# Optimization experiments

Measured on AMD Instinct MI355X. Metric: run time of the kernel, lower is better.

## Reference

```python
import jax, jax.numpy as jnp
import numpy as np

SPP_LEVELS = (4, 3, 2, 1)

def spp(x):
    # x: (N, C, H, W); H, W divisible by every level -> exact adaptive max pool
    N, C, H, W = x.shape
    feats = []
    for n in SPP_LEVELS:
        p = x.reshape(N, C, n, H // n, n, W // n).max(axis=(3, 5))  # (N,C,n,n)
        feats.append(p.reshape(N, -1))
    return jnp.concatenate(feats, axis=-1)  # (N, C*30) = (N, 90)

def lstm_cell(x, h, c, Wih, Whh, bih, bhh):
    g = Wih @ x + bih + Whh @ h + bhh
    i, f, gg, o = jnp.split(g, 4)
    i = jax.nn.sigmoid(i); f = jax.nn.sigmoid(f)
    gg = jnp.tanh(gg); o = jax.nn.sigmoid(o)
    c2 = f * c + i * gg
    return o * jnp.tanh(c2), c2

def setup_inputs() -> dict:
    key = jax.random.key(0)
    ks = jax.random.split(key, 16)
    E = 4096
    frames = jax.random.normal(ks[0], (1, 512, 3, 192, 192), dtype=jnp.float32)
    s = 0.02
    return {
        'frames': frames,
        'W_spp': jax.random.normal(ks[1], (E, 90), jnp.float32) * s,
        'b_spp': jnp.zeros((E,), jnp.float32),
        'W_fc7': jax.random.normal(ks[2], (64, E), jnp.float32) * s,
        'b_fc7': jnp.zeros((64,), jnp.float32),
        'W_fcast': jax.random.normal(ks[3], (64, E), jnp.float32) * s,
        'b_fcast': jnp.zeros((64,), jnp.float32),
        'Wih1': jax.random.normal(ks[4], (256, 64), jnp.float32) * s,
        'Whh1': jax.random.normal(ks[5], (256, 64), jnp.float32) * s,
        'bih1': jnp.zeros((256,), jnp.float32),
        'bhh1': jnp.zeros((256,), jnp.float32),
        'Wih2': jax.random.normal(ks[6], (128, 64), jnp.float32) * s,
        'Whh2': jax.random.normal(ks[7], (128, 32), jnp.float32) * s,
        'bih2': jnp.zeros((128,), jnp.float32),
        'bhh2': jnp.zeros((128,), jnp.float32),
        'W_fc8': jax.random.normal(ks[8], (1, 32), jnp.float32) * s,
        'b_fc8': jnp.zeros((1,), jnp.float32),
    }

def reference(frames, W_spp, b_spp, W_fc7, b_fc7, W_fcast, b_fcast,
              Wih1, Whh1, bih1, bhh1, Wih2, Whh2, bih2, bhh2, W_fc8, b_fc8):
    B, S, C, H, W = frames.shape  # B == 1 (module semantics require it)
    flat = frames.reshape(B * S, C, H, W)
    pooled = spp(flat)                                   # (S, 90)
    pooled = jax.nn.relu(pooled @ W_spp.T + b_spp)       # (S, 4096); dropout p=0
    embedded = jax.nn.relu(pooled @ W_fc7.T + b_fc7)     # (S, 64)
    fcast = jax.nn.relu(pooled @ W_fcast.T + b_fcast)    # (S, 64)

    def step(carry, xs):
        h1, c1, h2, c2 = carry
        x, fx = xs
        h1, c1 = lstm_cell(x, h1, c1, Wih1, Whh1, bih1, bhh1)
        h2, c2 = lstm_cell(h1, h2, c2, Wih2, Whh2, bih2, bhh2)
        # forecast branch: same cells with updated hidden, but state not kept
        fh1, _ = lstm_cell(fx, h1, c1, Wih1, Whh1, bih1, bhh1)
        fh2, _ = lstm_cell(fh1, h2, c2, Wih2, Whh2, bih2, bhh2)
        return (h1, c1, h2, c2), (h2, fh2)

    init = (jnp.zeros(64), jnp.zeros(64), jnp.zeros(32), jnp.zeros(32))
    _, (prog, fprog) = jax.lax.scan(step, init, (embedded, fcast))  # (S,32) each

    progress = jax.nn.sigmoid(prog @ W_fc8.T + b_fc8).reshape(B, S)
    forecasted = jax.nn.sigmoid(fprog @ W_fc8.T + b_fc8).reshape(B, S)
    return progress, forecasted
```

## Files before the change

### kernel.cpp

```cpp
#include <hip/hip_runtime.h>
#include <float.h>
#include <math.h>

__global__ __launch_bounds__(192) void spp_kernel(const float* __restrict__ frames,
                                                  float* __restrict__ pooled) {
    int bc = blockIdx.x;
    int w  = threadIdx.x;
    const float* img = frames + (size_t)bc * (192 * 192);

    float cm[12];
#pragma unroll
    for (int ch = 0; ch < 12; ++ch) {
        float m = -FLT_MAX;
#pragma unroll
        for (int r = 0; r < 16; ++r)
            m = fmaxf(m, img[(ch * 16 + r) * 192 + w]);
        cm[ch] = m;
    }

    __shared__ float band[10][192];
#pragma unroll
    for (int i = 0; i < 4; ++i)
        band[i][w] = fmaxf(fmaxf(cm[3*i], cm[3*i+1]), cm[3*i+2]);
#pragma unroll
    for (int i = 0; i < 3; ++i)
        band[4+i][w] = fmaxf(fmaxf(cm[4*i], cm[4*i+1]), fmaxf(cm[4*i+2], cm[4*i+3]));
#pragma unroll
    for (int i = 0; i < 2; ++i) {
        float m = cm[6*i];
#pragma unroll
        for (int k = 1; k < 6; ++k) m = fmaxf(m, cm[6*i+k]);
        band[7+i][w] = m;
    }
    {
        float m = cm[0];
#pragma unroll
        for (int k = 1; k < 12; ++k) m = fmaxf(m, cm[k]);
        band[9][w] = m;
    }
    __syncthreads();

    int s = bc / 3, c = bc % 3;
    float* orow = pooled + s * 90;
    int t = w;
    if (t < 16) {
        int r = t >> 2, cc = t & 3;
        float m = -FLT_MAX;
        for (int x = cc * 48; x < cc * 48 + 48; ++x) m = fmaxf(m, band[r][x]);
        orow[c * 16 + t] = m;
    } else if (t < 25) {
        int idx = t - 16, r = idx / 3, cc = idx % 3;
        float m = -FLT_MAX;
        for (int x = cc * 64; x < cc * 64 + 64; ++x) m = fmaxf(m, band[4 + r][x]);
        orow[48 + c * 9 + idx] = m;
    } else if (t < 29) {
        int idx = t - 25, r = idx >> 1, cc = idx & 1;
        float m = -FLT_MAX;
        for (int x = cc * 96; x < cc * 96 + 96; ++x) m = fmaxf(m, band[7 + r][x]);
        orow[75 + c * 4 + idx] = m;
    } else if (t == 29) {
        float m = -FLT_MAX;
        for (int x = 0; x < 192; ++x) m = fmaxf(m, band[9][x]);
        orow[87 + c] = m;
    }
}

__global__ __launch_bounds__(256) void fc_spp_kernel(const float* __restrict__ pooled,
                                                     const float* __restrict__ W,
                                                     const float* __restrict__ b,
                                                     float* __restrict__ out) {
    int ec = blockIdx.x;
    int fc = blockIdx.y;
    int t  = threadIdx.x;
    int s0 = fc * 8;

    __shared__ __align__(16) float sp[90 * 8];
    for (int i = t; i < 720; i += 256) {
        int j = i >> 3, f = i & 7;
        sp[i] = pooled[(s0 + f) * 90 + j];
    }
    __syncthreads();

    int e0 = ec * 1024 + t;
    float acc[4][8];
#pragma unroll
    for (int k = 0; k < 4; ++k) {
        float bb = b[e0 + k * 256];
#pragma unroll
        for (int f = 0; f < 8; ++f) acc[k][f] = bb;
    }
    for (int j = 0; j < 90; ++j) {
        float w0 = W[(e0 + 0 * 256) * 90 + j];
        float w1 = W[(e0 + 1 * 256) * 90 + j];
        float w2 = W[(e0 + 2 * 256) * 90 + j];
        float w3 = W[(e0 + 3 * 256) * 90 + j];
        float4 pa = *(const float4*)&sp[j * 8 + 0];
        float4 pb = *(const float4*)&sp[j * 8 + 4];
        float pv[8] = {pa.x, pa.y, pa.z, pa.w, pb.x, pb.y, pb.z, pb.w};
#pragma unroll
        for (int f = 0; f < 8; ++f) {
            acc[0][f] += w0 * pv[f];
            acc[1][f] += w1 * pv[f];
            acc[2][f] += w2 * pv[f];
            acc[3][f] += w3 * pv[f];
        }
    }
#pragma unroll
    for (int k = 0; k < 4; ++k)
#pragma unroll
        for (int f = 0; f < 8; ++f)
            out[(size_t)(s0 + f) * 4096 + e0 + k * 256] = fmaxf(acc[k][f], 0.f);
}

__global__ __launch_bounds__(512) void fc7cast_kernel(const float* __restrict__ prelu,
                                                      const float* __restrict__ W7,
                                                      const float* __restrict__ b7,
                                                      const float* __restrict__ Wc,
                                                      const float* __restrict__ bc,
                                                      float* __restrict__ emb,
                                                      float* __restrict__ fca) {
    int blk = blockIdx.x;
    int t   = threadIdx.x;
    int s0  = blk * 4;

    __shared__ __align__(16) float pr[4 * 4096];
    const float4* src = (const float4*)(prelu + (size_t)s0 * 4096);
    float4* dst = (float4*)pr;
    for (int i = t; i < 4096; i += 512) dst[i] = src[i];
    __syncthreads();

    int o = t & 127;
    int f = t >> 7;
    const float* wr;
    float bias;
    if (o < 64) { wr = W7 + (size_t)o * 4096; bias = b7[o]; }
    else        { wr = Wc + (size_t)(o - 64) * 4096; bias = bc[o - 64]; }

    const float4* w4 = (const float4*)wr;
    const float4* p4 = (const float4*)(pr + f * 4096);
    float a0 = 0.f, a1 = 0.f, a2 = 0.f, a3 = 0.f;
    for (int j = 0; j < 1024; ++j) {
        float4 wv = w4[j];
        float4 pv = p4[j];
        a0 += wv.x * pv.x; a1 += wv.y * pv.y;
        a2 += wv.z * pv.z; a3 += wv.w * pv.w;
    }
    float a = fmaxf(a0 + a1 + a2 + a3 + bias, 0.f);
    if (o < 64) emb[(s0 + f) * 64 + o] = a;
    else        fca[(s0 + f) * 64 + (o - 64)] = a;
}

__global__ __launch_bounds__(256) void pregate_kernel(const float* __restrict__ emb,
                                                      const float* __restrict__ fca,
                                                      const float* __restrict__ Wih1,
                                                      const float* __restrict__ bih1,
                                                      const float* __restrict__ bhh1,
                                                      float* __restrict__ gm,
                                                      float* __restrict__ gf) {
    int s = blockIdx.x;
    int t = threadIdx.x;
    __shared__ float x[64], fx[64];
    if (t < 64) x[t] = emb[s * 64 + t];
    else if (t < 128) fx[t - 64] = fca[s * 64 + (t - 64)];
    __syncthreads();

    const float* wr = Wih1 + t * 64;
    float am = bih1[t] + bhh1[t];
    float af = am;
#pragma unroll
    for (int j = 0; j < 64; ++j) {
        float w = wr[j];
        am += w * x[j];
        af += w * fx[j];
    }
    gm[s * 256 + t] = am;
    gf[s * 256 + t] = af;
}

__device__ __forceinline__ float sigf(float x) { return 1.f / (1.f + expf(-x)); }
__device__ __forceinline__ float act_fun(float x, int type) {
    return (type == 2) ? tanhf(x) : sigf(x);
}

__global__ __launch_bounds__(256) void lstm_main_kernel(const float* __restrict__ gm,
                                                        const float* __restrict__ Whh1,
                                                        const float* __restrict__ Wih2,
                                                        const float* __restrict__ Whh2,
                                                        const float* __restrict__ bih2,
                                                        const float* __restrict__ bhh2,
                                                        float* __restrict__ h1t,
                                                        float* __restrict__ c1t,
                                                        float* __restrict__ h2t,
                                                        float* __restrict__ c2t) {
    int t = threadIdx.x;

    __shared__ __align__(16) float h1s[64];
    __shared__ __align__(16) float h2s[32];
    __shared__ float act1[256];
    __shared__ float act2[128];
    __shared__ float act2p[128];

    float wh[64];
#pragma unroll
    for (int j = 0; j < 64; ++j) wh[j] = Whh1[t * 64 + j];

    float wu[64];
#pragma unroll
    for (int j = 0; j < 64; ++j) wu[j] = 0.f;
    float b2 = 0.f;
    if (t < 128) {
#pragma unroll
        for (int j = 0; j < 64; ++j) wu[j] = Wih2[t * 64 + j];
        b2 = bih2[t] + bhh2[t];
    } else {
#pragma unroll
        for (int j = 0; j < 32; ++j) wu[j] = Whh2[(t - 128) * 32 + j];
    }

    float c1r = 0.f;
    float c2r = 0.f;
    if (t < 64) h1s[t] = 0.f;
    if (t < 32) h2s[t] = 0.f;
    __syncthreads();

    float gmv = gm[t];

    for (int s = 0; s < 512; ++s) {
        float gnext = (s < 511) ? gm[(s + 1) * 256 + t] : 0.f;

        {
            float a0 = 0.f, a1 = 0.f, a2 = 0.f, a3 = 0.f;
#pragma unroll
            for (int j = 0; j < 16; ++j) {
                float4 h = ((const float4*)h1s)[j];
                a0 += wh[4*j+0] * h.x; a1 += wh[4*j+1] * h.y;
                a2 += wh[4*j+2] * h.z; a3 += wh[4*j+3] * h.w;
            }
            act1[t] = act_fun(gmv + ((a0 + a1) + (a2 + a3)), t >> 6);
        }
        gmv = gnext;
        __syncthreads();

        if (t < 64) {
            float iv = act1[t], fv = act1[64+t], gv = act1[128+t], ov = act1[192+t];
            float cn = fv * c1r + iv * gv;
            c1r = cn;
            float hn = ov * tanhf(cn);
            h1s[t] = hn;
            h1t[s * 64 + t] = hn;
            c1t[s * 64 + t] = cn;
        }
        __syncthreads();

        if (t < 128) {
            float a0 = b2, a1 = 0.f, a2 = 0.f, a3 = 0.f;
#pragma unroll
            for (int j = 0; j < 16; ++j) {
                float4 h = ((const float4*)h1s)[j];
                a0 += wu[4*j+0] * h.x; a1 += wu[4*j+1] * h.y;
                a2 += wu[4*j+2] * h.z; a3 += wu[4*j+3] * h.w;
            }
            act2[t] = (a0 + a1) + (a2 + a3);
        } else {
            float a0 = 0.f, a1 = 0.f, a2 = 0.f, a3 = 0.f;
#pragma unroll
            for (int j = 0; j < 8; ++j) {
                float4 h = ((const float4*)h2s)[j];
                a0 += wu[4*j+0] * h.x; a1 += wu[4*j+1] * h.y;
                a2 += wu[4*j+2] * h.z; a3 += wu[4*j+3] * h.w;
            }
            act2p[t - 128] = (a0 + a1) + (a2 + a3);
        }
        __syncthreads();

        if (t < 32) {
            float iv = sigf(act2[t]       + act2p[t]);
            float fv = sigf(act2[32 + t]  + act2p[32 + t]);
            float gv = tanhf(act2[64 + t] + act2p[64 + t]);
            float ov = sigf(act2[96 + t]  + act2p[96 + t]);
            float cn = fv * c2r + iv * gv;
            c2r = cn;
            float hn = ov * tanhf(cn);
            h2s[t] = hn;
            h2t[s * 32 + t] = hn;
            c2t[s * 32 + t] = cn;
        }
    }
}

__global__ __launch_bounds__(256) void forecast_kernel(const float* __restrict__ gf,
                                                       const float* __restrict__ Whh1,
                                                       const float* __restrict__ Wih2,
                                                       const float* __restrict__ Whh2,
                                                       const float* __restrict__ bih2,
                                                       const float* __restrict__ bhh2,
                                                       const float* __restrict__ h1t,
                                                       const float* __restrict__ c1t,
                                                       const float* __restrict__ h2t,
                                                       const float* __restrict__ c2t,
                                                       const float* __restrict__ Wfc8,
                                                       const float* __restrict__ bfc8,
                                                       float* __restrict__ out) {
    int s = blockIdx.x;
    int t = threadIdx.x;

    __shared__ __align__(16) float h1v[64];
    __shared__ __align__(16) float h2v[32];
    __shared__ __align__(16) float fh1[64];
    __shared__ float a1s[256];
    __shared__ float a2s[128];

    if (t < 64) h1v[t] = h1t[s * 64 + t];
    else if (t < 96) h2v[t - 64] = h2t[s * 32 + (t - 64)];
    __syncthreads();

    {
        const float* wr = Whh1 + t * 64;
        float a0 = 0.f, a1 = 0.f, a2 = 0.f, a3 = 0.f;
#pragma unroll
        for (int j = 0; j < 16; ++j) {
            float4 h = ((const float4*)h1v)[j];
            a0 += wr[4*j+0] * h.x; a1 += wr[4*j+1] * h.y;
            a2 += wr[4*j+2] * h.z; a3 += wr[4*j+3] * h.w;
        }
        a1s[t] = act_fun(gf[s * 256 + t] + ((a0 + a1) + (a2 + a3)), t >> 6);
    }
    __syncthreads();

    if (t < 64) {
        float iv = a1s[t], fv = a1s[64+t], gv = a1s[128+t], ov = a1s[192+t];
        float cf = fv * c1t[s * 64 + t] + iv * gv;
        fh1[t] = ov * tanhf(cf);
    }
    __syncthreads();

    if (t < 128) {
        const float* wi = Wih2 + t * 64;
        const float* wh = Whh2 + t * 32;
        float a0 = bih2[t] + bhh2[t], a1 = 0.f, a2 = 0.f, a3 = 0.f;
#pragma unroll
        for (int j = 0; j < 16; ++j) {
            float4 h = ((const float4*)fh1)[j];
            a0 += wi[4*j+0] * h.x; a1 += wi[4*j+1] * h.y;
            a2 += wi[4*j+2] * h.z; a3 += wi[4*j+3] * h.w;
        }
#pragma unroll
        for (int j = 0; j < 8; ++j) {
            float4 h = ((const float4*)h2v)[j];
            a0 += wh[4*j+0] * h.x; a1 += wh[4*j+1] * h.y;
            a2 += wh[4*j+2] * h.z; a3 += wh[4*j+3] * h.w;
        }
        a2s[t] = act_fun((a0 + a1) + (a2 + a3), (t >> 5) & 3);
    }
    __syncthreads();

    if (t < 64) {
        float pv = 0.f, fv2 = 0.f;
        if (t < 32) {
            float iv = a2s[t], fv = a2s[32+t], gv = a2s[64+t], ov = a2s[96+t];
            float cf2 = fv * c2t[s * 32 + t] + iv * gv;
            float fh2 = ov * tanhf(cf2);
            float w8 = Wfc8[t];
            pv  = w8 * h2v[t];
            fv2 = w8 * fh2;
        }
#pragma unroll
        for (int off = 16; off > 0; off >>= 1) {
            pv  += __shfl_xor(pv, off);
            fv2 += __shfl_xor(fv2, off);
        }
        if (t == 0) {
            float bf8 = bfc8[0];
            out[s]       = sigf(pv + bf8);
            out[512 + s] = sigf(fv2 + bf8);
        }
    }
}

extern "C" void kernel_launch(void* const* d_in, const int* in_sizes, int n_in,
                              void* d_out, int out_size, void* d_ws, size_t ws_size,
                              hipStream_t stream) {
    const float* frames  = (const float*)d_in[0];
    const float* W_spp   = (const float*)d_in[1];
    const float* b_spp   = (const float*)d_in[2];
    const float* W_fc7   = (const float*)d_in[3];
    const float* b_fc7   = (const float*)d_in[4];
    const float* W_fcast = (const float*)d_in[5];
    const float* b_fcast = (const float*)d_in[6];
    const float* Wih1    = (const float*)d_in[7];
    const float* Whh1    = (const float*)d_in[8];
    const float* bih1    = (const float*)d_in[9];
    const float* bhh1    = (const float*)d_in[10];
    const float* Wih2    = (const float*)d_in[11];
    const float* Whh2    = (const float*)d_in[12];
    const float* bih2    = (const float*)d_in[13];
    const float* bhh2    = (const float*)d_in[14];
    const float* W_fc8   = (const float*)d_in[15];
    const float* b_fc8   = (const float*)d_in[16];
    float* out = (float*)d_out;

    float* ws     = (float*)d_ws;
    float* pooled = ws;
    float* prelu  = pooled + 512 * 90;
    float* emb    = prelu + 512 * 4096;
    float* fca    = emb + 512 * 64;
    float* gm     = fca + 512 * 64;
    float* gf     = gm + 512 * 256;
    float* h1t    = gf + 512 * 256;
    float* c1t    = h1t + 512 * 64;
    float* h2t    = c1t + 512 * 64;
    float* c2t    = h2t + 512 * 32;

    spp_kernel<<<1536, 192, 0, stream>>>(frames, pooled);
    fc_spp_kernel<<<dim3(4, 64), 256, 0, stream>>>(pooled, W_spp, b_spp, prelu);
    fc7cast_kernel<<<128, 512, 0, stream>>>(prelu, W_fc7, b_fc7, W_fcast, b_fcast, emb, fca);
    pregate_kernel<<<512, 256, 0, stream>>>(emb, fca, Wih1, bih1, bhh1, gm, gf);
    lstm_main_kernel<<<1, 256, 0, stream>>>(gm, Whh1, Wih2, Whh2, bih2, bhh2,
                                            h1t, c1t, h2t, c2t);
    forecast_kernel<<<512, 256, 0, stream>>>(gf, Whh1, Wih2, Whh2, bih2, bhh2,
                                             h1t, c1t, h2t, c2t, W_fc8, b_fc8, out);
}
```

Baseline: 1.290 ms.

## Replicate LSTM state across waves with readlane broadcasts and fewer barriers

The sequential LSTM kernel now keeps h1/h2 and c1/c2 replicated in registers in every wave and broadcasts hidden values with readlane instead of going through shared memory. This cuts the per-step barriers from four to two, using raw s_barrier calls. Fast rcp/exp-based sigmoid and tanh replace expf/tanhf everywhere, trading some accuracy for latency. The SPP kernel switches to float4 loads with a shared-memory column-max stage.

```diff
diff --git a/kernel.cpp b/kernel.cpp
--- a/kernel.cpp
+++ b/kernel.cpp
@@ -2,66 +2,83 @@
 #include <float.h>
 #include <math.h>
 
+__device__ __forceinline__ float fsig(float x) {
+    return __builtin_amdgcn_rcpf(1.f + __expf(-x));
+}
+__device__ __forceinline__ float ftanh(float x) {
+    return 1.f - 2.f * __builtin_amdgcn_rcpf(1.f + __expf(2.f * x));
+}
+__device__ __forceinline__ float fact(float x, int type) {
+    return (type == 2) ? ftanh(x) : fsig(x);
+}
+__device__ __forceinline__ float rdlane(float v, int j) {
+    return __int_as_float(__builtin_amdgcn_readlane(__float_as_int(v), j));
+}
+
 __global__ __launch_bounds__(192) void spp_kernel(const float* __restrict__ frames,
                                                   float* __restrict__ pooled) {
     int bc = blockIdx.x;
-    int w  = threadIdx.x;
-    const float* img = frames + (size_t)bc * (192 * 192);
-
-    float cm[12];
-#pragma unroll
-    for (int ch = 0; ch < 12; ++ch) {
-        float m = -FLT_MAX;
-#pragma unroll
-        for (int r = 0; r < 16; ++r)
-            m = fmaxf(m, img[(ch * 16 + r) * 192 + w]);
-        cm[ch] = m;
-    }
+    int t  = threadIdx.x;
+    int q  = t / 48;
+    int c  = t % 48;
+    const float4* img4 = (const float4*)(frames + (size_t)bc * (192 * 192));
+
+    __shared__ float cmall[12][192];
+#pragma unroll
+    for (int k = 0; k < 3; ++k) {
+        int ch = 3 * q + k;
+        float4 m = img4[(ch * 16) * 48 + c];
+#pragma unroll
+        for (int r = 1; r < 16; ++r) {
+            float4 v = img4[(ch * 16 + r) * 48 + c];
+            m.x = fmaxf(m.x, v.x); m.y = fmaxf(m.y, v.y);
+            m.z = fmaxf(m.z, v.z); m.w = fmaxf(m.w, v.w);
+        }
+        cmall[ch][4 * c + 0] = m.x; cmall[ch][4 * c + 1] = m.y;
+        cmall[ch][4 * c + 2] = m.z; cmall[ch][4 * c + 3] = m.w;
+    }
+    __syncthreads();
 
     __shared__ float band[10][192];
+    int w = t;
 #pragma unroll
     for (int i = 0; i < 4; ++i)
-        band[i][w] = fmaxf(fmaxf(cm[3*i], cm[3*i+1]), cm[3*i+2]);
+        band[i][w] = fmaxf(fmaxf(cmall[3*i][w], cmall[3*i+1][w]), cmall[3*i+2][w]);
 #pragma unroll
     for (int i = 0; i < 3; ++i)
-        band[4+i][w] = fmaxf(fmaxf(cm[4*i], cm[4*i+1]), fmaxf(cm[4*i+2], cm[4*i+3]));
+        band[4+i][w] = fmaxf(fmaxf(cmall[4*i][w], cmall[4*i+1][w]),
+                             fmaxf(cmall[4*i+2][w], cmall[4*i+3][w]));
 #pragma unroll
     for (int i = 0; i < 2; ++i) {
-        float m = cm[6*i];
-#pragma unroll
-        for (int k = 1; k < 6; ++k) m = fmaxf(m, cm[6*i+k]);
+        float m = cmall[6*i][w];
+#pragma unroll
+        for (int k = 1; k < 6; ++k) m = fmaxf(m, cmall[6*i+k][w]);
         band[7+i][w] = m;
     }
-    {
-        float m = cm[0];
-#pragma unroll
-        for (int k = 1; k < 12; ++k) m = fmaxf(m, cm[k]);
-        band[9][w] = m;
-    }
-    __syncthreads();
-
-    int s = bc / 3, c = bc % 3;
+    band[9][w] = fmaxf(band[7][w], band[8][w]);
+    __syncthreads();
+
+    int s = bc / 3, cch = bc % 3;
     float* orow = pooled + s * 90;
-    int t = w;
     if (t < 16) {
         int r = t >> 2, cc = t & 3;
         float m = -FLT_MAX;
         for (int x = cc * 48; x < cc * 48 + 48; ++x) m = fmaxf(m, band[r][x]);
-        orow[c * 16 + t] = m;
+        orow[cch * 16 + t] = m;
     } else if (t < 25) {
         int idx = t - 16, r = idx / 3, cc = idx % 3;
         float m = -FLT_MAX;
         for (int x = cc * 64; x < cc * 64 + 64; ++x) m = fmaxf(m, band[4 + r][x]);
-        orow[48 + c * 9 + idx] = m;
+        orow[48 + cch * 9 + idx] = m;
     } else if (t < 29) {
         int idx = t - 25, r = idx >> 1, cc = idx & 1;
         float m = -FLT_MAX;
         for (int x = cc * 96; x < cc * 96 + 96; ++x) m = fmaxf(m, band[7 + r][x]);
-        orow[75 + c * 4 + idx] = m;
+        orow[75 + cch * 4 + idx] = m;
     } else if (t == 29) {
         float m = -FLT_MAX;
         for (int x = 0; x < 192; ++x) m = fmaxf(m, band[9][x]);
-        orow[87 + c] = m;
+        orow[87 + cch] = m;
     }
 }
 
@@ -177,36 +194,28 @@
     gf[s * 256 + t] = af;
 }
 
-__device__ __forceinline__ float sigf(float x) { return 1.f / (1.f + expf(-x)); }
-__device__ __forceinline__ float act_fun(float x, int type) {
-    return (type == 2) ? tanhf(x) : sigf(x);
-}
-
-__global__ __launch_bounds__(256) void lstm_main_kernel(const float* __restrict__ gm,
-                                                        const float* __restrict__ Whh1,
-                                                        const float* __restrict__ Wih2,
-                                                        const float* __restrict__ Whh2,
-                                                        const float* __restrict__ bih2,
-                                                        const float* __restrict__ bhh2,
-                                                        float* __restrict__ h1t,
-                                                        float* __restrict__ c1t,
-                                                        float* __restrict__ h2t,
-                                                        float* __restrict__ c2t) {
-    int t = threadIdx.x;
-
-    __shared__ __align__(16) float h1s[64];
-    __shared__ __align__(16) float h2s[32];
+__global__ __launch_bounds__(256, 1) void lstm_main_kernel(
+    const float* __restrict__ gm,
+    const float* __restrict__ Whh1,
+    const float* __restrict__ Wih2,
+    const float* __restrict__ Whh2,
+    const float* __restrict__ bih2,
+    const float* __restrict__ bhh2,
+    float* __restrict__ h1t, float* __restrict__ c1t,
+    float* __restrict__ h2t, float* __restrict__ c2t)
+{
+    const int t  = threadIdx.x;
+    const int l  = t & 63;
+    const int wv = t >> 6;
+
     __shared__ float act1[256];
-    __shared__ float act2[128];
-    __shared__ float act2p[128];
+    __shared__ float part2[256];
 
     float wh[64];
 #pragma unroll
     for (int j = 0; j < 64; ++j) wh[j] = Whh1[t * 64 + j];
 
     float wu[64];
-#pragma unroll
-    for (int j = 0; j < 64; ++j) wu[j] = 0.f;
     float b2 = 0.f;
     if (t < 128) {
 #pragma unroll
@@ -215,75 +224,83 @@
     } else {
 #pragma unroll
         for (int j = 0; j < 32; ++j) wu[j] = Whh2[(t - 128) * 32 + j];
-    }
-
-    float c1r = 0.f;
-    float c2r = 0.f;
-    if (t < 64) h1s[t] = 0.f;
-    if (t < 32) h2s[t] = 0.f;
-    __syncthreads();
-
+#pragma unroll
+        for (int j = 32; j < 64; ++j) wu[j] = 0.f;
+    }
+
+    float h1r = 0.f, c1r = 0.f;
+    float h2r = 0.f, c2r = 0.f;
     float gmv = gm[t];
 
     for (int s = 0; s < 512; ++s) {
-        float gnext = (s < 511) ? gm[(s + 1) * 256 + t] : 0.f;
+        float gnx = (s < 511) ? gm[(s + 1) * 256 + t] : 0.f;
 
         {
-            float a0 = 0.f, a1 = 0.f, a2 = 0.f, a3 = 0.f;
-#pragma unroll
-            for (int j = 0; j < 16; ++j) {
-                float4 h = ((const float4*)h1s)[j];
-                a0 += wh[4*j+0] * h.x; a1 += wh[4*j+1] * h.y;
-                a2 += wh[4*j+2] * h.z; a3 += wh[4*j+3] * h.w;
+            float a0 = gmv, a1 = 0.f, a2 = 0.f, a3 = 0.f;
+#pragma unroll
+            for (int j = 0; j < 64; j += 4) {
+                a0 += wh[j]     * rdlane(h1r, j);
+                a1 += wh[j + 1] * rdlane(h1r, j + 1);
+                a2 += wh[j + 2] * rdlane(h1r, j + 2);
+                a3 += wh[j + 3] * rdlane(h1r, j + 3);
             }
-            act1[t] = act_fun(gmv + ((a0 + a1) + (a2 + a3)), t >> 6);
-        }
-        gmv = gnext;
-        __syncthreads();
-
-        if (t < 64) {
-            float iv = act1[t], fv = act1[64+t], gv = act1[128+t], ov = act1[192+t];
-            float cn = fv * c1r + iv * gv;
-            c1r = cn;
-            float hn = ov * tanhf(cn);
-            h1s[t] = hn;
-            h1t[s * 64 + t] = hn;
-            c1t[s * 64 + t] = cn;
-        }
-        __syncthreads();
+            act1[t] = fact((a0 + a1) + (a2 + a3), t >> 6);
+        }
+        gmv = gnx;
+        asm volatile("s_waitcnt lgkmcnt(0)" ::: "memory");
+        __builtin_amdgcn_s_barrier();
+
+        {
+            float iv = act1[l], fv = act1[64 + l], gv = act1[128 + l], ov = act1[192 + l];
+            c1r = fv * c1r + iv * gv;
+            h1r = ov * ftanh(c1r);
+            if (wv == 0) {
+                h1t[s * 64 + l] = h1r;
+                c1t[s * 64 + l] = c1r;
+            }
+        }
 
         if (t < 128) {
-            float a0 = b2, a1 = 0.f, a2 = 0.f, a3 = 0.f;
-#pragma unroll
-            for (int j = 0; j < 16; ++j) {
-                float4 h = ((const float4*)h1s)[j];
-                a0 += wu[4*j+0] * h.x; a1 += wu[4*j+1] * h.y;
-                a2 += wu[4*j+2] * h.z; a3 += wu[4*j+3] * h.w;
+            float p0 = b2, p1 = 0.f, p2 = 0.f, p3 = 0.f;
+#pragma unroll
+            for (int j = 0; j < 64; j += 4) {
+                p0 += wu[j]     * rdlane(h1r, j);
+                p1 += wu[j + 1] * rdlane(h1r, j + 1);
+                p2 += wu[j + 2] * rdlane(h1r, j + 2);
+                p3 += wu[j + 3] * rdlane(h1r, j + 3);
             }
-            act2[t] = (a0 + a1) + (a2 + a3);
+            part2[2 * t] = (p0 + p1) + (p2 + p3);
         } else {
-            float a0 = 0.f, a1 = 0.f, a2 = 0.f, a3 = 0.f;
-#pragma unroll
-            for (int j = 0; j < 8; ++j) {
-                float4 h = ((const float4*)h2s)[j];
-                a0 += wu[4*j+0] * h.x; a1 += wu[4*j+1] * h.y;
-                a2 += wu[4*j+2] * h.z; a3 += wu[4*j+3] * h.w;
+            int u = t - 128;
+            float p0 = 0.f, p1 = 0.f, p2 = 0.f, p3 = 0.f;
+#pragma unroll
+            for (int k = 0; k < 32; k += 4) {
+                p0 += wu[k]     * rdlane(h2r, k);
+                p1 += wu[k + 1] * rdlane(h2r, k + 1);
+                p2 += wu[k + 2] * rdlane(h2r, k + 2);
+                p3 += wu[k + 3] * rdlane(h2r, k + 3);
             }
-            act2p[t - 128] = (a0 + a1) + (a2 + a3);
-        }
-        __syncthreads();
-
-        if (t < 32) {
-            float iv = sigf(act2[t]       + act2p[t]);
-            float fv = sigf(act2[32 + t]  + act2p[32 + t]);
-            float gv = tanhf(act2[64 + t] + act2p[64 + t]);
-            float ov = sigf(act2[96 + t]  + act2p[96 + t]);
-            float cn = fv * c2r + iv * gv;
-            c2r = cn;
-            float hn = ov * tanhf(cn);
-            h2s[t] = hn;
-            h2t[s * 32 + t] = hn;
-            c2t[s * 32 + t] = cn;
+            part2[2 * u + 1] = (p0 + p1) + (p2 + p3);
+        }
+        asm volatile("s_waitcnt lgkmcnt(0)" ::: "memory");
+        __builtin_amdgcn_s_barrier();
+
+        {
+            int k = l & 31;
+            float2 pi = *(const float2*)&part2[2 * k];
+            float2 pf = *(const float2*)&part2[2 * (32 + k)];
+            float2 pg = *(const float2*)&part2[2 * (64 + k)];
+            float2 po = *(const float2*)&part2[2 * (96 + k)];
+            float iv = fsig(pi.x + pi.y);
+            float fv = fsig(pf.x + pf.y);
+            float gv = ftanh(pg.x + pg.y);
+            float ov = fsig(po.x + po.y);
+            c2r = fv * c2r + iv * gv;
+            h2r = ov * ftanh(c2r);
+            if (wv == 0 && l < 32) {
+                h2t[s * 32 + k] = h2r;
+                c2t[s * 32 + k] = c2r;
+            }
         }
     }
 }
@@ -323,14 +340,14 @@
             a0 += wr[4*j+0] * h.x; a1 += wr[4*j+1] * h.y;
             a2 += wr[4*j+2] * h.z; a3 += wr[4*j+3] * h.w;
         }
-        a1s[t] = act_fun(gf[s * 256 + t] + ((a0 + a1) + (a2 + a3)), t >> 6);
+        a1s[t] = fact(gf[s * 256 + t] + ((a0 + a1) + (a2 + a3)), t >> 6);
     }
     __syncthreads();
 
     if (t < 64) {
         float iv = a1s[t], fv = a1s[64+t], gv = a1s[128+t], ov = a1s[192+t];
         float cf = fv * c1t[s * 64 + t] + iv * gv;
-        fh1[t] = ov * tanhf(cf);
+        fh1[t] = ov * ftanh(cf);
     }
     __syncthreads();
 
@@ -350,7 +367,7 @@
             a0 += wh[4*j+0] * h.x; a1 += wh[4*j+1] * h.y;
             a2 += wh[4*j+2] * h.z; a3 += wh[4*j+3] * h.w;
         }
-        a2s[t] = act_fun((a0 + a1) + (a2 + a3), (t >> 5) & 3);
+        a2s[t] = fact((a0 + a1) + (a2 + a3), (t >> 5) & 3);
     }
     __syncthreads();
 
@@ -359,7 +376,7 @@
         if (t < 32) {
             float iv = a2s[t], fv = a2s[32+t], gv = a2s[64+t], ov = a2s[96+t];
             float cf2 = fv * c2t[s * 32 + t] + iv * gv;
-            float fh2 = ov * tanhf(cf2);
+            float fh2 = ov * ftanh(cf2);
             float w8 = Wfc8[t];
             pv  = w8 * h2v[t];
             fv2 = w8 * fh2;
@@ -371,8 +388,8 @@
         }
         if (t == 0) {
             float bf8 = bfc8[0];
-            out[s]       = sigf(pv + bf8);
-            out[512 + s] = sigf(fv2 + bf8);
+            out[s]       = fsig(pv + bf8);
+            out[512 + s] = fsig(fv2 + bf8);
         }
     }
 }
```

After: 1.318 ms. 2.2% more time.
